# Kernel optimization log

Measured on AMD Instinct MI355X. Metric: run time of the kernel, lower is better.

The kernel has to match this reference:

```python
import jax, jax.numpy as jnp
import numpy as np

B, S, D, M = 4, 1024, 128, 20000
THRESH = 0.1          # memory.query_with_indices threshold
CW_MIN = 0.01         # compound_weight > 0.01 gate
TI_MIN = 0.01         # total_influence > 0.01 gate
NORM_EPS = 1e-6       # norm_sq > 1e-6 gate
INF_EPS = 1e-5        # division epsilon


def setup_inputs() -> dict:
    key = jax.random.key(0)
    ks = jax.random.split(key, 4)
    sd = 1.0 / np.sqrt(D)
    return {
        "input_tensor": jax.random.normal(ks[0], (B, S, D), dtype=jnp.float32),
        "mem": jax.random.normal(ks[1], (M, D), dtype=jnp.float32),
        "W1": jax.random.normal(ks[2], (D, D), dtype=jnp.float32) * sd,
        "b1": jnp.zeros((D,), dtype=jnp.float32),
        "ln_g": jnp.ones((D,), dtype=jnp.float32),
        "ln_b": jnp.zeros((D,), dtype=jnp.float32),
        "W2": jax.random.normal(ks[3], (D, D), dtype=jnp.float32) * sd,
        "b2": jnp.zeros((D,), dtype=jnp.float32),
    }


def reference(input_tensor, mem, W1, b1, ln_g, ln_b, W2, b2):
    x = input_tensor  # [B,S,D]
    # fusion_net: Linear -> LayerNorm -> ReLU
    h = jnp.einsum("bsd,ed->bse", x, W1) + b1
    mu = h.mean(-1, keepdims=True)
    var = h.var(-1, keepdims=True)
    h = (h - mu) * jax.lax.rsqrt(var + 1e-5) * ln_g + ln_b
    feats = jax.nn.relu(h)
    raw = jnp.einsum("bsd,ed->bse", feats, W2) + b2  # [B,S,D]

    # GraphMemory query: cosine similarity, keep entries with sim > THRESH
    xn = x * jax.lax.rsqrt(jnp.sum(x * x, -1, keepdims=True) + 1e-12)
    mn = mem * jax.lax.rsqrt(jnp.sum(mem * mem, -1, keepdims=True) + 1e-12)
    sim = jnp.einsum("bsd,md->bsm", xn, mn)              # [B,S,M]
    w = jnp.where(sim > THRESH, sim, 0.0)                # per-token weights

    # compound_weight per batch & memory slot (sum over seq positions)
    cw = w.sum(axis=1)                                   # [B,M]
    norm_sq = jnp.sum(mem * mem, -1)                     # [M]
    active = (cw > CW_MIN) & (norm_sq > NORM_EPS)        # [B,M]
    eff = jnp.where(active, cw, 0.0)                     # effective weights

    # projection of each target vec onto each memory vec
    safe_ns = jnp.where(norm_sq > NORM_EPS, norm_sq, 1.0)
    coef = jnp.einsum("bsd,md->bsm", raw, mem) / safe_ns # [B,S,M]
    correction = jnp.einsum("bsm,bm,md->bsd", coef, eff, mem)  # [B,S,D]

    ti = eff.sum(-1)                                     # [B] total_influence
    corr = correction / (ti + INF_EPS)[:, None, None]
    final = jnp.where((ti > TI_MIN)[:, None, None], raw + 0.5 * corr, raw)
    return final
```

## Files before the change

### kernel.cpp

```cpp
#include <hip/hip_runtime.h>

#define DD 128
#define SS 1024
#define BB 4
#define M_TOT 20000
#define M_PAD 20480
#define GM_NCH 64
#define GM_CH 320
#define FMLP_BLOCKS 128
#define PREP_BLOCKS 320

typedef __bf16 bf16x8 __attribute__((ext_vector_type(8)));
typedef unsigned short u16x8 __attribute__((ext_vector_type(8)));
typedef float f32x16 __attribute__((ext_vector_type(16)));

union BF8 { bf16x8 b; u16x8 u; };

__device__ __forceinline__ unsigned short f2bf(float f) {
    unsigned int u = __float_as_uint(f);
    u += 0x7FFFu + ((u >> 16) & 1u);
    return (unsigned short)(u >> 16);
}
__device__ __forceinline__ float bf2f(unsigned short h) {
    return __uint_as_float(((unsigned int)h) << 16);
}

__global__ __launch_bounds__(256) void k_front(
    const float* __restrict__ x, const float* __restrict__ W1,
    const float* __restrict__ b1, const float* __restrict__ ln_g,
    const float* __restrict__ ln_b, const float* __restrict__ W2,
    const float* __restrict__ b2, const float* __restrict__ mem,
    unsigned short* __restrict__ xnb, float* __restrict__ raw,
    unsigned short* __restrict__ mnb, unsigned short* __restrict__ mnT,
    float* __restrict__ norm_sq, float* __restrict__ ti,
    float* __restrict__ cw) {
    __shared__ __align__(16) char smem_raw[64 * 136 * 2];
    const int tid = threadIdx.x;
    const int bid = blockIdx.x;

    if (bid < FMLP_BLOCKS) {
        unsigned short* featsL = (unsigned short*)smem_raw;
        float* redp = (float*)(smem_raw + 8704);
        float2* stats = (float2*)(smem_raw + 8704 + 1024);
        const int lane = tid & 63, wv = tid >> 6;
        const int col = lane & 31, hi = lane >> 5;
        const int t0 = bid * 32;
        const int ct = wv;

        bf16x8 Af[8];
        float sq = 0.f;
        const float* xrow = x + (size_t)(t0 + col) * DD + hi * 8;
        #pragma unroll
        for (int kk = 0; kk < 8; ++kk) {
            float4 p = *(const float4*)(xrow + kk * 16);
            float4 q = *(const float4*)(xrow + kk * 16 + 4);
            BF8 t;
            t.u[0] = f2bf(p.x); t.u[1] = f2bf(p.y); t.u[2] = f2bf(p.z); t.u[3] = f2bf(p.w);
            t.u[4] = f2bf(q.x); t.u[5] = f2bf(q.y); t.u[6] = f2bf(q.z); t.u[7] = f2bf(q.w);
            Af[kk] = t.b;
            sq += p.x * p.x + p.y * p.y + p.z * p.z + p.w * p.w;
            sq += q.x * q.x + q.y * q.y + q.z * q.z + q.w * q.w;
        }
        sq += __shfl_xor(sq, 32);
        float xrs = rsqrtf(sq + 1e-12f);
        if (wv == 0) {
            unsigned short* xo = xnb + (size_t)(t0 + col) * DD + hi * 8;
            #pragma unroll
            for (int kk = 0; kk < 8; ++kk) {
                BF8 t; t.b = Af[kk];
                u16x8 o;
                #pragma unroll
                for (int j = 0; j < 8; ++j) o[j] = f2bf(bf2f(t.u[j]) * xrs);
                *(u16x8*)(xo + kk * 16) = o;
            }
        }

        f32x16 acc;
        {
            float bv = b1[ct * 32 + col];
            #pragma unroll
            for (int r = 0; r < 16; ++r) acc[r] = bv;
        }
        const float* w1row = W1 + (size_t)(ct * 32 + col) * DD + hi * 8;
        #pragma unroll
        for (int kk = 0; kk < 8; ++kk) {
            float4 p = *(const float4*)(w1row + kk * 16);
            float4 q = *(const float4*)(w1row + kk * 16 + 4);
            BF8 t;
            t.u[0] = f2bf(p.x); t.u[1] = f2bf(p.y); t.u[2] = f2bf(p.z); t.u[3] = f2bf(p.w);
            t.u[4] = f2bf(q.x); t.u[5] = f2bf(q.y); t.u[6] = f2bf(q.z); t.u[7] = f2bf(q.w);
            acc = __builtin_amdgcn_mfma_f32_32x32x16_bf16(Af[kk], t.b, acc, 0, 0, 0);
        }

        float rs_[16], rq_[16];
        #pragma unroll
        for (int r = 0; r < 16; ++r) { float v = acc[r]; rs_[r] = v; rq_[r] = v * v; }
        #pragma unroll
        for (int off = 1; off < 32; off <<= 1) {
            #pragma unroll
            for (int r = 0; r < 16; ++r) {
                rs_[r] += __shfl_xor(rs_[r], off);
                rq_[r] += __shfl_xor(rq_[r], off);
            }
        }
        if (col == 0) {
            #pragma unroll
            for (int r = 0; r < 16; ++r) {
                int row = (r & 3) + 8 * (r >> 2) + 4 * hi;
                redp[(wv * 32 + row) * 2 + 0] = rs_[r];
                redp[(wv * 32 + row) * 2 + 1] = rq_[r];
            }
        }
        __syncthreads();
        if (tid < 32) {
            float S = redp[(0 * 32 + tid) * 2] + redp[(1 * 32 + tid) * 2] +
                      redp[(2 * 32 + tid) * 2] + redp[(3 * 32 + tid) * 2];
            float Q = redp[(0 * 32 + tid) * 2 + 1] + redp[(1 * 32 + tid) * 2 + 1] +
                      redp[(2 * 32 + tid) * 2 + 1] + redp[(3 * 32 + tid) * 2 + 1];
            float mu = S * (1.f / 128.f);
            float rstd = rsqrtf(Q * (1.f / 128.f) - mu * mu + 1e-5f);
            stats[tid] = make_float2(mu, rstd);
        }
        __syncthreads();

        {
            float gv = ln_g[ct * 32 + col], bv = ln_b[ct * 32 + col];
            #pragma unroll
            for (int r = 0; r < 16; ++r) {
                int row = (r & 3) + 8 * (r >> 2) + 4 * hi;
                float2 st = stats[row];
                float v = fmaxf((acc[r] - st.x) * st.y * gv + bv, 0.f);
                featsL[row * 136 + ct * 32 + col] = f2bf(v);
            }
        }
        __syncthreads();

        f32x16 a2;
        {
            float bv = b2[ct * 32 + col];
            #pragma unroll
            for (int r = 0; r < 16; ++r) a2[r] = bv;
        }
        const float* w2row = W2 + (size_t)(ct * 32 + col) * DD + hi * 8;
        #pragma unroll
        for (int kk = 0; kk < 8; ++kk) {
            bf16x8 Aq = *(const bf16x8*)&featsL[(lane & 31) * 136 + hi * 8 + kk * 16];
            float4 p = *(const float4*)(w2row + kk * 16);
            float4 q = *(const float4*)(w2row + kk * 16 + 4);
            BF8 t;
            t.u[0] = f2bf(p.x); t.u[1] = f2bf(p.y); t.u[2] = f2bf(p.z); t.u[3] = f2bf(p.w);
            t.u[4] = f2bf(q.x); t.u[5] = f2bf(q.y); t.u[6] = f2bf(q.z); t.u[7] = f2bf(q.w);
            a2 = __builtin_amdgcn_mfma_f32_32x32x16_bf16(Aq, t.b, a2, 0, 0, 0);
        }
        #pragma unroll
        for (int r = 0; r < 16; ++r) {
            int row = (r & 3) + 8 * (r >> 2) + 4 * hi;
            raw[(size_t)(t0 + row) * DD + ct * 32 + col] = a2[r];
        }
    } else {
        unsigned short* RM = (unsigned short*)smem_raw;
        const int pb = bid - FMLP_BLOCKS;
        const int m0 = pb * 64;
        cw[pb * 256 + tid] = 0.0f;
        if (pb == 0 && tid < BB) ti[tid] = 0.0f;

        const int r = tid >> 2, seg = tid & 3;
        const int m = m0 + r;
        const bool ok = m < M_TOT;
        float4 v[8];
        const float4* src = (const float4*)mem + (size_t)m * 32 + seg * 8;
        #pragma unroll
        for (int i = 0; i < 8; ++i)
            v[i] = ok ? src[i] : make_float4(0.f, 0.f, 0.f, 0.f);
        float ss = 0.f;
        #pragma unroll
        for (int i = 0; i < 8; ++i)
            ss += v[i].x * v[i].x + v[i].y * v[i].y + v[i].z * v[i].z + v[i].w * v[i].w;
        ss += __shfl_xor(ss, 1);
        ss += __shfl_xor(ss, 2);
        float rs = rsqrtf(ss + 1e-12f);
        if (seg == 0) norm_sq[m] = ss;

        #pragma unroll
        for (int i = 0; i < 4; ++i) {
            float4 a = v[2 * i], bq = v[2 * i + 1];
            u16x8 o;
            o[0] = f2bf(a.x * rs); o[1] = f2bf(a.y * rs);
            o[2] = f2bf(a.z * rs); o[3] = f2bf(a.w * rs);
            o[4] = f2bf(bq.x * rs); o[5] = f2bf(bq.y * rs);
            o[6] = f2bf(bq.z * rs); o[7] = f2bf(bq.w * rs);
            *(u16x8*)(mnb + (size_t)m * DD + seg * 32 + i * 8) = o;
            *(u16x8*)(RM + r * 136 + seg * 32 + i * 8) = o;
        }
        __syncthreads();
        const int d = tid >> 1, half = tid & 1;
        unsigned short* dst = mnT + (size_t)d * M_PAD + m0 + half * 32;
        #pragma unroll
        for (int q = 0; q < 4; ++q) {
            u16x8 o;
            #pragma unroll
            for (int j = 0; j < 8; ++j)
                o[j] = RM[(half * 32 + q * 8 + j) * 136 + d];
            *(u16x8*)(dst + q * 8) = o;
        }
    }
}

__global__ __launch_bounds__(256, 3) void k_cw(
    const unsigned short* __restrict__ xnb, const unsigned short* __restrict__ mnb,
    float* __restrict__ cw) {
    __shared__ unsigned short As[2][32 * 128];
    const int tid = threadIdx.x, lane = tid & 63, wv = tid >> 6;
    const int c = lane & 31, h = lane >> 5;
    const int b = blockIdx.z;
    const int mw = blockIdx.x * 256 + wv * 64;
    const int s_base = blockIdx.y * 256;

    const int srow = tid >> 4, sk16 = tid & 15;
    const int soff = srow * 128 + ((sk16 * 8) ^ ((srow & 15) << 3));
    const int srow1 = (tid + 256) >> 4;
    const int soff1 = srow1 * 128 + ((sk16 * 8) ^ ((srow1 & 15) << 3));
    const unsigned short* xbase = xnb + ((size_t)b * SS + s_base) * DD;

    bf16x8 Bf[2][8];
    #pragma unroll
    for (int ct = 0; ct < 2; ++ct)
        #pragma unroll
        for (int kk = 0; kk < 8; ++kk)
            Bf[ct][kk] = *(const bf16x8*)(mnb + (size_t)(mw + ct * 32 + c) * DD +
                                          kk * 16 + h * 8);

    {
        u16x8 v0 = *(const u16x8*)(xbase + (size_t)srow * DD + sk16 * 8);
        u16x8 v1 = *(const u16x8*)(xbase + (size_t)srow1 * DD + sk16 * 8);
        *(u16x8*)&As[0][soff] = v0;
        *(u16x8*)&As[0][soff1] = v1;
    }

    float cw0 = 0.f, cw1 = 0.f;
    #pragma unroll 1
    for (int it = 0; it < 8; ++it) {
        __syncthreads();
        u16x8 v0, v1;
        if (it < 7) {
            const unsigned short* nb = xbase + (size_t)(it + 1) * 32 * DD;
            v0 = *(const u16x8*)(nb + (size_t)srow * DD + sk16 * 8);
            v1 = *(const u16x8*)(nb + (size_t)srow1 * DD + sk16 * 8);
        }
        f32x16 p0, p1;
        #pragma unroll
        for (int r = 0; r < 16; ++r) { p0[r] = 0.f; p1[r] = 0.f; }
        const unsigned short* Ab = As[it & 1];
        __builtin_amdgcn_s_setprio(1);
        #pragma unroll
        for (int kk = 0; kk < 8; ++kk) {
            bf16x8 Afr = *(const bf16x8*)&Ab[c * 128 + ((kk * 16 + h * 8) ^ ((c & 15) << 3))];
            p0 = __builtin_amdgcn_mfma_f32_32x32x16_bf16(Afr, Bf[0][kk], p0, 0, 0, 0);
            p1 = __builtin_amdgcn_mfma_f32_32x32x16_bf16(Afr, Bf[1][kk], p1, 0, 0, 0);
        }
        __builtin_amdgcn_s_setprio(0);
        if (it < 7) {
            unsigned short* An = As[(it + 1) & 1];
            *(u16x8*)&An[soff] = v0;
            *(u16x8*)&An[soff1] = v1;
        }
        #pragma unroll
        for (int r = 0; r < 16; ++r) {
            float a = p0[r], bb = p1[r];
            cw0 += a > 0.1f ? a : 0.f;
            cw1 += bb > 0.1f ? bb : 0.f;
        }
    }
    cw0 += __shfl_xor(cw0, 32);
    cw1 += __shfl_xor(cw1, 32);
    if (lane < 32) {
        atomicAdd(&cw[(size_t)b * M_PAD + mw + c], cw0);
        atomicAdd(&cw[(size_t)b * M_PAD + mw + 32 + c], cw1);
    }
}

__global__ __launch_bounds__(256) void k_gmatm(
    const unsigned short* __restrict__ mnT, const float* __restrict__ cw,
    const float* __restrict__ norm_sq, float* __restrict__ ti,
    float* __restrict__ pG) {
    __shared__ float effL[GM_CH];
    __shared__ float rb[4];
    const int tid = threadIdx.x, lane = tid & 63, wv = tid >> 6;
    const int c = lane & 31, h = lane >> 5;
    const int b = blockIdx.y;
    const int m0 = blockIdx.x * GM_CH;

    float tsum = 0.f;
    #pragma unroll
    for (int idx = tid; idx < GM_CH; idx += 256) {
        int m = m0 + idx;
        float e = 0.f;
        if (m < M_TOT) {
            float cc = cw[(size_t)b * M_PAD + m];
            float ns = norm_sq[m];
            e = (cc > 0.01f && ns > 1e-6f) ? cc : 0.f;
        }
        effL[idx] = e;
        tsum += e;
    }
    #pragma unroll
    for (int off = 1; off < 64; off <<= 1) tsum += __shfl_xor(tsum, off);
    if (lane == 0) rb[wv] = tsum;
    __syncthreads();
    if (tid == 0) atomicAdd(&ti[b], rb[0] + rb[1] + rb[2] + rb[3]);

    f32x16 a0, a1, a2, a3;
    #pragma unroll
    for (int r = 0; r < 16; ++r) { a0[r] = 0.f; a1[r] = 0.f; a2[r] = 0.f; a3[r] = 0.f; }

    const unsigned short* Arow = mnT + (size_t)(wv * 32 + c) * M_PAD;
    const unsigned short* B0r = mnT + (size_t)(0 * 32 + c) * M_PAD;
    const unsigned short* B1r = mnT + (size_t)(1 * 32 + c) * M_PAD;
    const unsigned short* B2r = mnT + (size_t)(2 * 32 + c) * M_PAD;
    const unsigned short* B3r = mnT + (size_t)(3 * 32 + c) * M_PAD;

    #pragma unroll 1
    for (int t = 0; t < GM_CH / 64; ++t) {
        #pragma unroll
        for (int kk = 0; kk < 4; ++kk) {
            const int mo = m0 + t * 64 + kk * 16 + h * 8;
            const int eo = t * 64 + kk * 16 + h * 8;
            u16x8 au = *(const u16x8*)(Arow + mo);
            float4 e0 = *(float4*)&effL[eo];
            float4 e1 = *(float4*)&effL[eo + 4];
            BF8 af;
            af.u[0] = f2bf(bf2f(au[0]) * e0.x);
            af.u[1] = f2bf(bf2f(au[1]) * e0.y);
            af.u[2] = f2bf(bf2f(au[2]) * e0.z);
            af.u[3] = f2bf(bf2f(au[3]) * e0.w);
            af.u[4] = f2bf(bf2f(au[4]) * e1.x);
            af.u[5] = f2bf(bf2f(au[5]) * e1.y);
            af.u[6] = f2bf(bf2f(au[6]) * e1.z);
            af.u[7] = f2bf(bf2f(au[7]) * e1.w);
            bf16x8 B0 = *(const bf16x8*)(B0r + mo);
            bf16x8 B1 = *(const bf16x8*)(B1r + mo);
            bf16x8 B2 = *(const bf16x8*)(B2r + mo);
            bf16x8 B3 = *(const bf16x8*)(B3r + mo);
            a0 = __builtin_amdgcn_mfma_f32_32x32x16_bf16(af.b, B0, a0, 0, 0, 0);
            a1 = __builtin_amdgcn_mfma_f32_32x32x16_bf16(af.b, B1, a1, 0, 0, 0);
            a2 = __builtin_amdgcn_mfma_f32_32x32x16_bf16(af.b, B2, a2, 0, 0, 0);
            a3 = __builtin_amdgcn_mfma_f32_32x32x16_bf16(af.b, B3, a3, 0, 0, 0);
        }
    }
    float* o = pG + (size_t)(blockIdx.x * BB + b) * (DD * DD);
    #pragma unroll
    for (int r = 0; r < 16; ++r) {
        int rf = (r & 3) + 8 * (r >> 2) + 4 * h;
        o[(wv * 32 + rf) * DD + 0 * 32 + c] = a0[r];
        o[(wv * 32 + rf) * DD + 1 * 32 + c] = a1[r];
        o[(wv * 32 + rf) * DD + 2 * 32 + c] = a2[r];
        o[(wv * 32 + rf) * DD + 3 * 32 + c] = a3[r];
    }
}

__global__ __launch_bounds__(256) void k_gmat2(const float* __restrict__ pG,
                                               float* __restrict__ G) {
    __shared__ float4 redv[256];
    const int tid = threadIdx.x;
    const int b = blockIdx.y;
    const int f4i = blockIdx.x * 64 + (tid & 63);
    const int cg = tid >> 6;
    const float4* pG4 = (const float4*)pG;
    float4 s = make_float4(0.f, 0.f, 0.f, 0.f);
    for (int c = cg; c < GM_NCH; c += 4) {
        float4 p = pG4[(size_t)(c * BB + b) * (DD * DD / 4) + f4i];
        s.x += p.x; s.y += p.y; s.z += p.z; s.w += p.w;
    }
    redv[tid] = s;
    __syncthreads();
    if (tid < 64) {
        float4 r0 = redv[tid], r1 = redv[tid + 64], r2 = redv[tid + 128], r3 = redv[tid + 192];
        float4 o = make_float4(r0.x + r1.x + r2.x + r3.x, r0.y + r1.y + r2.y + r3.y,
                               r0.z + r1.z + r2.z + r3.z, r0.w + r1.w + r2.w + r3.w);
        ((float4*)G)[(size_t)b * (DD * DD / 4) + f4i] = o;
    }
}

__global__ __launch_bounds__(256) void k_final(
    const float* __restrict__ raw, const float* __restrict__ Gmat,
    const float* __restrict__ ti, float* __restrict__ out) {
    __shared__ float Gl[DD * DD];
    __shared__ float rawl[32 * DD];
    const int tid = threadIdx.x;
    const int b = blockIdx.y;
    const int s0 = blockIdx.x * 32;
    const float4* Gv = (const float4*)(Gmat + (size_t)b * DD * DD);
    #pragma unroll
    for (int i = 0; i < 16; ++i) ((float4*)Gl)[tid + i * 256] = Gv[tid + i * 256];
    const float4* rv = (const float4*)(raw + ((size_t)b * SS + s0) * DD);
    #pragma unroll
    for (int i = 0; i < 4; ++i) ((float4*)rawl)[tid + i * 256] = rv[tid + i * 256];
    __syncthreads();
    float tib = ti[b];
    float scale = (tib > 0.01f) ? 0.5f / (tib + 1e-5f) : 0.0f;
    const int dq = tid & 31;
    const int sg = tid >> 5;
    const float4* Gl4 = (const float4*)Gl;
    #pragma unroll 1
    for (int t = 0; t < 4; ++t) {
        int s = sg + t * 8;
        float4 acc = make_float4(0.f, 0.f, 0.f, 0.f);
        #pragma unroll
        for (int k = 0; k < DD; ++k) {
            float r = rawl[s * DD + k];
            float4 gv = Gl4[k * 32 + dq];
            acc.x += r * gv.x; acc.y += r * gv.y;
            acc.z += r * gv.z; acc.w += r * gv.w;
        }
        float4 rw = ((const float4*)rawl)[s * 32 + dq];
        float4 o = make_float4(rw.x + scale * acc.x, rw.y + scale * acc.y,
                               rw.z + scale * acc.z, rw.w + scale * acc.w);
        ((float4*)(out + ((size_t)b * SS + s0) * DD))[s * 32 + dq] = o;
    }
}

extern "C" void kernel_launch(void* const* d_in, const int* in_sizes, int n_in,
                              void* d_out, int out_size, void* d_ws, size_t ws_size,
                              hipStream_t stream) {
    const float* x   = (const float*)d_in[0];
    const float* mem = (const float*)d_in[1];
    const float* W1  = (const float*)d_in[2];
    const float* b1  = (const float*)d_in[3];
    const float* lg  = (const float*)d_in[4];
    const float* lb  = (const float*)d_in[5];
    const float* W2  = (const float*)d_in[6];
    const float* b2  = (const float*)d_in[7];
    float* out = (float*)d_out;

    float* wsf = (float*)d_ws;
    size_t off = 0;
    unsigned short* mnb = (unsigned short*)(wsf + off); off += (size_t)M_PAD * 64;
    unsigned short* mnT = (unsigned short*)(wsf + off); off += (size_t)M_PAD * 64;
    float* norm_sq = wsf + off;                         off += M_PAD;
    unsigned short* xnb = (unsigned short*)(wsf + off); off += (size_t)BB * SS * 64;
    float* raw = wsf + off;                             off += (size_t)BB * SS * DD;
    float* cw  = wsf + off;                             off += (size_t)BB * M_PAD;
    float* G   = wsf + off;                             off += (size_t)BB * DD * DD;
    float* ti  = wsf + off;                             off += BB;
    float* pG  = wsf + off;                             off += (size_t)GM_NCH * BB * DD * DD;

    k_front<<<dim3(FMLP_BLOCKS + PREP_BLOCKS), 256, 0, stream>>>(
        x, W1, b1, lg, lb, W2, b2, mem, xnb, raw, mnb, mnT, norm_sq, ti, cw);
    k_cw<<<dim3(M_PAD / 256, 4, BB), 256, 0, stream>>>(xnb, mnb, cw);
    k_gmatm<<<dim3(GM_NCH, BB), 256, 0, stream>>>(mnT, cw, norm_sq, ti, pG);
    k_gmat2<<<dim3(DD * DD / 256, BB), 256, 0, stream>>>(pG, G);
    k_final<<<dim3(SS / 32, BB), 256, 0, stream>>>(raw, G, ti, out);
}
```

Baseline: 81.72 us.

## Use MFMA in final GEMM, split gram-matrix blocks, deepen k_cw prefetch

k_final switches from an fp32 scalar FMA loop over an LDS-resident G to bf16 MFMA. G is now stored as bf16 by k_gmat2 and raw is converted to bf16 in registers, so k_final no longer needs the 64 KB LDS staging. k_gmatm splits each output tile across two blocks per batch, giving more parallelism with fewer accumulators per wave. k_cw uses a four-buffer LDS ring and prefetches two 32-row tiles per sync. Rounding G and raw to bf16 in the correction term lowers its precision.

```diff
diff --git a/kernel.cpp b/kernel.cpp
--- a/kernel.cpp
+++ b/kernel.cpp
@@ -209,7 +209,7 @@
 __global__ __launch_bounds__(256, 3) void k_cw(
     const unsigned short* __restrict__ xnb, const unsigned short* __restrict__ mnb,
     float* __restrict__ cw) {
-    __shared__ unsigned short As[2][32 * 128];
+    __shared__ unsigned short As[4][32 * 128];
     const int tid = threadIdx.x, lane = tid & 63, wv = tid >> 6;
     const int c = lane & 31, h = lane >> 5;
     const int b = blockIdx.z;
@@ -218,7 +218,7 @@
 
     const int srow = tid >> 4, sk16 = tid & 15;
     const int soff = srow * 128 + ((sk16 * 8) ^ ((srow & 15) << 3));
-    const int srow1 = (tid + 256) >> 4;
+    const int srow1 = srow + 16;
     const int soff1 = srow1 * 128 + ((sk16 * 8) ^ ((srow1 & 15) << 3));
     const unsigned short* xbase = xnb + ((size_t)b * SS + s_base) * DD;
 
@@ -231,44 +231,73 @@
                                           kk * 16 + h * 8);
 
     {
-        u16x8 v0 = *(const u16x8*)(xbase + (size_t)srow * DD + sk16 * 8);
-        u16x8 v1 = *(const u16x8*)(xbase + (size_t)srow1 * DD + sk16 * 8);
-        *(u16x8*)&As[0][soff] = v0;
-        *(u16x8*)&As[0][soff1] = v1;
+        u16x8 a0 = *(const u16x8*)(xbase + (size_t)srow * DD + sk16 * 8);
+        u16x8 a1 = *(const u16x8*)(xbase + (size_t)srow1 * DD + sk16 * 8);
+        const unsigned short* n1 = xbase + (size_t)32 * DD;
+        u16x8 b0 = *(const u16x8*)(n1 + (size_t)srow * DD + sk16 * 8);
+        u16x8 b1 = *(const u16x8*)(n1 + (size_t)srow1 * DD + sk16 * 8);
+        *(u16x8*)&As[0][soff] = a0; *(u16x8*)&As[0][soff1] = a1;
+        *(u16x8*)&As[1][soff] = b0; *(u16x8*)&As[1][soff1] = b1;
     }
 
     float cw0 = 0.f, cw1 = 0.f;
     #pragma unroll 1
-    for (int it = 0; it < 8; ++it) {
+    for (int p = 0; p < 4; ++p) {
         __syncthreads();
-        u16x8 v0, v1;
-        if (it < 7) {
-            const unsigned short* nb = xbase + (size_t)(it + 1) * 32 * DD;
-            v0 = *(const u16x8*)(nb + (size_t)srow * DD + sk16 * 8);
-            v1 = *(const u16x8*)(nb + (size_t)srow1 * DD + sk16 * 8);
-        }
-        f32x16 p0, p1;
-        #pragma unroll
-        for (int r = 0; r < 16; ++r) { p0[r] = 0.f; p1[r] = 0.f; }
-        const unsigned short* Ab = As[it & 1];
-        __builtin_amdgcn_s_setprio(1);
-        #pragma unroll
-        for (int kk = 0; kk < 8; ++kk) {
-            bf16x8 Afr = *(const bf16x8*)&Ab[c * 128 + ((kk * 16 + h * 8) ^ ((c & 15) << 3))];
-            p0 = __builtin_amdgcn_mfma_f32_32x32x16_bf16(Afr, Bf[0][kk], p0, 0, 0, 0);
-            p1 = __builtin_amdgcn_mfma_f32_32x32x16_bf16(Afr, Bf[1][kk], p1, 0, 0, 0);
-        }
-        __builtin_amdgcn_s_setprio(0);
-        if (it < 7) {
-            unsigned short* An = As[(it + 1) & 1];
-            *(u16x8*)&An[soff] = v0;
-            *(u16x8*)&An[soff1] = v1;
-        }
-        #pragma unroll
-        for (int r = 0; r < 16; ++r) {
-            float a = p0[r], bb = p1[r];
-            cw0 += a > 0.1f ? a : 0.f;
-            cw1 += bb > 0.1f ? bb : 0.f;
+        u16x8 w0, w1, w2, w3;
+        if (p < 3) {
+            const unsigned short* n0 = xbase + (size_t)(2 * p + 2) * 32 * DD;
+            const unsigned short* n1 = xbase + (size_t)(2 * p + 3) * 32 * DD;
+            w0 = *(const u16x8*)(n0 + (size_t)srow * DD + sk16 * 8);
+            w1 = *(const u16x8*)(n0 + (size_t)srow1 * DD + sk16 * 8);
+            w2 = *(const u16x8*)(n1 + (size_t)srow * DD + sk16 * 8);
+            w3 = *(const u16x8*)(n1 + (size_t)srow1 * DD + sk16 * 8);
+        }
+        {
+            f32x16 p0, p1;
+            #pragma unroll
+            for (int r = 0; r < 16; ++r) { p0[r] = 0.f; p1[r] = 0.f; }
+            const unsigned short* Ab = As[(2 * p) & 3];
+            __builtin_amdgcn_s_setprio(1);
+            #pragma unroll
+            for (int kk = 0; kk < 8; ++kk) {
+                bf16x8 Afr = *(const bf16x8*)&Ab[c * 128 + ((kk * 16 + h * 8) ^ ((c & 15) << 3))];
+                p0 = __builtin_amdgcn_mfma_f32_32x32x16_bf16(Afr, Bf[0][kk], p0, 0, 0, 0);
+                p1 = __builtin_amdgcn_mfma_f32_32x32x16_bf16(Afr, Bf[1][kk], p1, 0, 0, 0);
+            }
+            __builtin_amdgcn_s_setprio(0);
+            #pragma unroll
+            for (int r = 0; r < 16; ++r) {
+                float a = p0[r], bb = p1[r];
+                cw0 += a > 0.1f ? a : 0.f;
+                cw1 += bb > 0.1f ? bb : 0.f;
+            }
+        }
+        {
+            f32x16 p0, p1;
+            #pragma unroll
+            for (int r = 0; r < 16; ++r) { p0[r] = 0.f; p1[r] = 0.f; }
+            const unsigned short* Ab = As[(2 * p + 1) & 3];
+            __builtin_amdgcn_s_setprio(1);
+            #pragma unroll
+            for (int kk = 0; kk < 8; ++kk) {
+                bf16x8 Afr = *(const bf16x8*)&Ab[c * 128 + ((kk * 16 + h * 8) ^ ((c & 15) << 3))];
+                p0 = __builtin_amdgcn_mfma_f32_32x32x16_bf16(Afr, Bf[0][kk], p0, 0, 0, 0);
+                p1 = __builtin_amdgcn_mfma_f32_32x32x16_bf16(Afr, Bf[1][kk], p1, 0, 0, 0);
+            }
+            __builtin_amdgcn_s_setprio(0);
+            if (p < 3) {
+                unsigned short* An0 = As[(2 * p + 2) & 3];
+                unsigned short* An1 = As[(2 * p + 3) & 3];
+                *(u16x8*)&An0[soff] = w0; *(u16x8*)&An0[soff1] = w1;
+                *(u16x8*)&An1[soff] = w2; *(u16x8*)&An1[soff1] = w3;
+            }
+            #pragma unroll
+            for (int r = 0; r < 16; ++r) {
+                float a = p0[r], bb = p1[r];
+                cw0 += a > 0.1f ? a : 0.f;
+                cw1 += bb > 0.1f ? bb : 0.f;
+            }
         }
     }
     cw0 += __shfl_xor(cw0, 32);
@@ -287,7 +316,8 @@
     __shared__ float rb[4];
     const int tid = threadIdx.x, lane = tid & 63, wv = tid >> 6;
     const int c = lane & 31, h = lane >> 5;
-    const int b = blockIdx.y;
+    const int half = blockIdx.y;
+    const int b = blockIdx.z;
     const int m0 = blockIdx.x * GM_CH;
 
     float tsum = 0.f;
@@ -307,17 +337,18 @@
     for (int off = 1; off < 64; off <<= 1) tsum += __shfl_xor(tsum, off);
     if (lane == 0) rb[wv] = tsum;
     __syncthreads();
-    if (tid == 0) atomicAdd(&ti[b], rb[0] + rb[1] + rb[2] + rb[3]);
-
-    f32x16 a0, a1, a2, a3;
-    #pragma unroll
-    for (int r = 0; r < 16; ++r) { a0[r] = 0.f; a1[r] = 0.f; a2[r] = 0.f; a3[r] = 0.f; }
-
-    const unsigned short* Arow = mnT + (size_t)(wv * 32 + c) * M_PAD;
-    const unsigned short* B0r = mnT + (size_t)(0 * 32 + c) * M_PAD;
-    const unsigned short* B1r = mnT + (size_t)(1 * 32 + c) * M_PAD;
-    const unsigned short* B2r = mnT + (size_t)(2 * 32 + c) * M_PAD;
-    const unsigned short* B3r = mnT + (size_t)(3 * 32 + c) * M_PAD;
+    if (half == 0 && tid == 0) atomicAdd(&ti[b], rb[0] + rb[1] + rb[2] + rb[3]);
+
+    const int rbase = half * 64 + (wv >> 1) * 32;
+    const int ct0 = (wv & 1) * 2;
+
+    f32x16 a0, a1;
+    #pragma unroll
+    for (int r = 0; r < 16; ++r) { a0[r] = 0.f; a1[r] = 0.f; }
+
+    const unsigned short* Arow = mnT + (size_t)(rbase + c) * M_PAD;
+    const unsigned short* B0r = mnT + (size_t)((ct0 + 0) * 32 + c) * M_PAD;
+    const unsigned short* B1r = mnT + (size_t)((ct0 + 1) * 32 + c) * M_PAD;
 
     #pragma unroll 1
     for (int t = 0; t < GM_CH / 64; ++t) {
@@ -339,27 +370,21 @@
             af.u[7] = f2bf(bf2f(au[7]) * e1.w);
             bf16x8 B0 = *(const bf16x8*)(B0r + mo);
             bf16x8 B1 = *(const bf16x8*)(B1r + mo);
-            bf16x8 B2 = *(const bf16x8*)(B2r + mo);
-            bf16x8 B3 = *(const bf16x8*)(B3r + mo);
             a0 = __builtin_amdgcn_mfma_f32_32x32x16_bf16(af.b, B0, a0, 0, 0, 0);
             a1 = __builtin_amdgcn_mfma_f32_32x32x16_bf16(af.b, B1, a1, 0, 0, 0);
-            a2 = __builtin_amdgcn_mfma_f32_32x32x16_bf16(af.b, B2, a2, 0, 0, 0);
-            a3 = __builtin_amdgcn_mfma_f32_32x32x16_bf16(af.b, B3, a3, 0, 0, 0);
         }
     }
     float* o = pG + (size_t)(blockIdx.x * BB + b) * (DD * DD);
     #pragma unroll
     for (int r = 0; r < 16; ++r) {
         int rf = (r & 3) + 8 * (r >> 2) + 4 * h;
-        o[(wv * 32 + rf) * DD + 0 * 32 + c] = a0[r];
-        o[(wv * 32 + rf) * DD + 1 * 32 + c] = a1[r];
-        o[(wv * 32 + rf) * DD + 2 * 32 + c] = a2[r];
-        o[(wv * 32 + rf) * DD + 3 * 32 + c] = a3[r];
+        o[(rbase + rf) * DD + (ct0 + 0) * 32 + c] = a0[r];
+        o[(rbase + rf) * DD + (ct0 + 1) * 32 + c] = a1[r];
     }
 }
 
 __global__ __launch_bounds__(256) void k_gmat2(const float* __restrict__ pG,
-                                               float* __restrict__ G) {
+                                               unsigned short* __restrict__ Gb) {
     __shared__ float4 redv[256];
     const int tid = threadIdx.x;
     const int b = blockIdx.y;
@@ -375,47 +400,51 @@
     __syncthreads();
     if (tid < 64) {
         float4 r0 = redv[tid], r1 = redv[tid + 64], r2 = redv[tid + 128], r3 = redv[tid + 192];
-        float4 o = make_float4(r0.x + r1.x + r2.x + r3.x, r0.y + r1.y + r2.y + r3.y,
-                               r0.z + r1.z + r2.z + r3.z, r0.w + r1.w + r2.w + r3.w);
-        ((float4*)G)[(size_t)b * (DD * DD / 4) + f4i] = o;
+        ushort4 o;
+        o.x = f2bf(r0.x + r1.x + r2.x + r3.x);
+        o.y = f2bf(r0.y + r1.y + r2.y + r3.y);
+        o.z = f2bf(r0.z + r1.z + r2.z + r3.z);
+        o.w = f2bf(r0.w + r1.w + r2.w + r3.w);
+        *(ushort4*)&Gb[(size_t)b * (DD * DD) + f4i * 4] = o;
     }
 }
 
 __global__ __launch_bounds__(256) void k_final(
-    const float* __restrict__ raw, const float* __restrict__ Gmat,
+    const float* __restrict__ raw, const unsigned short* __restrict__ Gb,
     const float* __restrict__ ti, float* __restrict__ out) {
-    __shared__ float Gl[DD * DD];
-    __shared__ float rawl[32 * DD];
-    const int tid = threadIdx.x;
-    const int b = blockIdx.y;
-    const int s0 = blockIdx.x * 32;
-    const float4* Gv = (const float4*)(Gmat + (size_t)b * DD * DD);
-    #pragma unroll
-    for (int i = 0; i < 16; ++i) ((float4*)Gl)[tid + i * 256] = Gv[tid + i * 256];
-    const float4* rv = (const float4*)(raw + ((size_t)b * SS + s0) * DD);
-    #pragma unroll
-    for (int i = 0; i < 4; ++i) ((float4*)rawl)[tid + i * 256] = rv[tid + i * 256];
-    __syncthreads();
+    const int tid = threadIdx.x, lane = tid & 63, wv = tid >> 6;
+    const int col = lane & 31, hi = lane >> 5;
+    const int t0 = blockIdx.x * 32;
+    const int b = blockIdx.x >> 5;
+    const int ct = wv;
+
+    bf16x8 Af[8];
+    const float* rrow = raw + (size_t)(t0 + col) * DD + hi * 8;
+    #pragma unroll
+    for (int kk = 0; kk < 8; ++kk) {
+        float4 p = *(const float4*)(rrow + kk * 16);
+        float4 q = *(const float4*)(rrow + kk * 16 + 4);
+        BF8 t;
+        t.u[0] = f2bf(p.x); t.u[1] = f2bf(p.y); t.u[2] = f2bf(p.z); t.u[3] = f2bf(p.w);
+        t.u[4] = f2bf(q.x); t.u[5] = f2bf(q.y); t.u[6] = f2bf(q.z); t.u[7] = f2bf(q.w);
+        Af[kk] = t.b;
+    }
+    f32x16 acc;
+    #pragma unroll
+    for (int r = 0; r < 16; ++r) acc[r] = 0.f;
+    const unsigned short* grow = Gb + (size_t)b * DD * DD + (size_t)(ct * 32 + col) * DD + hi * 8;
+    #pragma unroll
+    for (int kk = 0; kk < 8; ++kk) {
+        bf16x8 Bw = *(const bf16x8*)(grow + kk * 16);
+        acc = __builtin_amdgcn_mfma_f32_32x32x16_bf16(Af[kk], Bw, acc, 0, 0, 0);
+    }
     float tib = ti[b];
     float scale = (tib > 0.01f) ? 0.5f / (tib + 1e-5f) : 0.0f;
-    const int dq = tid & 31;
-    const int sg = tid >> 5;
-    const float4* Gl4 = (const float4*)Gl;
-    #pragma unroll 1
-    for (int t = 0; t < 4; ++t) {
-        int s = sg + t * 8;
-        float4 acc = make_float4(0.f, 0.f, 0.f, 0.f);
-        #pragma unroll
-        for (int k = 0; k < DD; ++k) {
-            float r = rawl[s * DD + k];
-            float4 gv = Gl4[k * 32 + dq];
-            acc.x += r * gv.x; acc.y += r * gv.y;
-            acc.z += r * gv.z; acc.w += r * gv.w;
-        }
-        float4 rw = ((const float4*)rawl)[s * 32 + dq];
-        float4 o = make_float4(rw.x + scale * acc.x, rw.y + scale * acc.y,
-                               rw.z + scale * acc.z, rw.w + scale * acc.w);
-        ((float4*)(out + ((size_t)b * SS + s0) * DD))[s * 32 + dq] = o;
+    #pragma unroll
+    for (int r = 0; r < 16; ++r) {
+        int row = (r & 3) + 8 * (r >> 2) + 4 * hi;
+        size_t idx = (size_t)(t0 + row) * DD + ct * 32 + col;
+        out[idx] = raw[idx] + scale * acc[r];
     }
 }
 
@@ -440,14 +469,14 @@
     unsigned short* xnb = (unsigned short*)(wsf + off); off += (size_t)BB * SS * 64;
     float* raw = wsf + off;                             off += (size_t)BB * SS * DD;
     float* cw  = wsf + off;                             off += (size_t)BB * M_PAD;
-    float* G   = wsf + off;                             off += (size_t)BB * DD * DD;
+    unsigned short* Gb = (unsigned short*)(wsf + off);  off += (size_t)BB * DD * DD / 2;
     float* ti  = wsf + off;                             off += BB;
     float* pG  = wsf + off;                             off += (size_t)GM_NCH * BB * DD * DD;
 
     k_front<<<dim3(FMLP_BLOCKS + PREP_BLOCKS), 256, 0, stream>>>(
         x, W1, b1, lg, lb, W2, b2, mem, xnb, raw, mnb, mnT, norm_sq, ti, cw);
     k_cw<<<dim3(M_PAD / 256, 4, BB), 256, 0, stream>>>(xnb, mnb, cw);
-    k_gmatm<<<dim3(GM_NCH, BB), 256, 0, stream>>>(mnT, cw, norm_sq, ti, pG);
-    k_gmat2<<<dim3(DD * DD / 256, BB), 256, 0, stream>>>(pG, G);
-    k_final<<<dim3(SS / 32, BB), 256, 0, stream>>>(raw, G, ti, out);
-}
+    k_gmatm<<<dim3(GM_NCH, 2, BB), 256, 0, stream>>>(mnT, cw, norm_sq, ti, pG);
+    k_gmat2<<<dim3(DD * DD / 256, BB), 256, 0, stream>>>(pG, Gb);
+    k_final<<<dim3(SS * BB / 32), 256, 0, stream>>>(raw, Gb, ti, out);
+}
```

After: 78.48 us. 4.0% less time.
